# Performance work log

Hardware: AMD Instinct MI355X
Metric: run time of the kernel (lower is better)

## Reference

```python
import jax, jax.numpy as jnp
import numpy as np

B, C, W = 32, 3, 512
KSIZE = 5
EPS = 8.0
ID_OFFSET = 4.0
SCALE = ID_OFFSET / (W - 1)            # identity_offset / (image_crop - 1)
DEF_OFF = (2.0 + SCALE) / 2.0          # deforming_offset
PIX_W = 2.0 / W                        # pixel width in [-1,1] coords

def _gauss_kernel2d(k):
    sigma = k * 0.15 + 0.35
    half = (k - 1) * 0.5
    x = np.linspace(-half, half, k)
    pdf = np.exp(-0.5 * (x / sigma) ** 2)
    k1 = pdf / pdf.sum()
    return np.outer(k1, k1).astype(np.float32)

def _samp_iden():
    seq = np.arange(-(W - 1), W, 2) / (W - 1.0)   # length W, identity coords
    gx = np.tile(seq, (W, 1))
    gy = gx.T
    return jnp.asarray(np.stack([gx, gy])[None].astype(np.float32))  # [1,2,W,W]

IDEN = _samp_iden()
GKER = jnp.broadcast_to(jnp.asarray(_gauss_kernel2d(KSIZE))[None, None], (2, 1, KSIZE, KSIZE))

def _blur(g):
    p = KSIZE // 2
    g = jnp.pad(g, ((0, 0), (0, 0), (p, p), (p, p)), mode='reflect')
    # depthwise conv over the 2 grid channels (groups=2)
    return jax.lax.conv_general_dilated(g, GKER, (1, 1), 'VALID', feature_group_count=2)

def _forward_grid(prim_grid):
    pg = _blur(prim_grid)
    sg = pg + IDEN                                   # prim -> samp
    # samp -> accu: conv_transpose with [1,-1] == first difference (leading zero)
    s = sg + DEF_OFF
    sx, sy = s[:, :1], s[:, 1:2]
    ax = sx - jnp.concatenate([jnp.zeros_like(sx[..., :1]), sx[..., :-1]], axis=3)
    ay = sy - jnp.concatenate([jnp.zeros_like(sy[:, :, :1]), sy[:, :, :-1]], axis=2)
    ag = jnp.concatenate([ax, ay], axis=1) / SCALE
    ag = jax.nn.relu(ag)                             # accu_clip
    # accu -> samp: conv_transpose with all-ones filter == cumulative sum
    a = ag * SCALE
    sx2 = jnp.cumsum(a[:, :1], axis=3)
    sy2 = jnp.cumsum(a[:, 1:2], axis=2)
    sg = jnp.concatenate([sx2, sy2], axis=1) - DEF_OFF
    pg = jnp.clip(sg - IDEN, -PIX_W * EPS, PIX_W * EPS)  # prim_clip
    return jnp.clip(pg + IDEN, -1.0, 1.0)                # samp_clip (hardtanh)

def _grid_sample(img, grid):
    # img [B,C,W,W], grid [B,W,W,2] in [-1,1]; bilinear, zeros padding, align_corners=True
    x = (grid[..., 0] + 1.0) * 0.5 * (W - 1)
    y = (grid[..., 1] + 1.0) * 0.5 * (W - 1)
    x0 = jnp.floor(x); y0 = jnp.floor(y)
    x1 = x0 + 1.0;     y1 = y0 + 1.0
    wx1 = x - x0; wx0 = 1.0 - wx1
    wy1 = y - y0; wy0 = 1.0 - wy1
    def gather(xi, yi):
        valid = ((xi >= 0) & (xi < W) & (yi >= 0) & (yi < W)).astype(img.dtype)
        xc = jnp.clip(xi, 0, W - 1).astype(jnp.int32)
        yc = jnp.clip(yi, 0, W - 1).astype(jnp.int32)
        v = jax.vmap(lambda im, yy, xx: im[:, yy, xx])(img, yc, xc)  # [B,C,W,W]
        return v * valid[:, None]
    return (gather(x0, y0) * (wx0 * wy0)[:, None] + gather(x1, y0) * (wx1 * wy0)[:, None]
          + gather(x0, y1) * (wx0 * wy1)[:, None] + gather(x1, y1) * (wx1 * wy1)[:, None])

def setup_inputs() -> dict:
    key = jax.random.key(0)
    k1, k2 = jax.random.split(key)
    image = jax.random.normal(k1, (B, C, W, W), dtype=jnp.float32)
    prim_grid = jax.random.normal(k2, (B, 2, W, W), dtype=jnp.float32) * 0.01
    return {"image": image, "prim_grid": prim_grid}

def reference(image, prim_grid):
    samp_grid = _forward_grid(prim_grid)
    binding_grid = jnp.transpose(samp_grid, (0, 2, 3, 1))  # [B,W,W,2]
    return _grid_sample(image, binding_grid)
```

## Files before the change

kernel.cpp:

```cpp
#include <hip/hip_runtime.h>
#include <math.h>

#define WID 512
#define NB  32
#define NC  3
#define WW  (WID * WID)

constexpr float SCALE_F   = (float)(4.0 / 511.0);
constexpr float DEF_OFF_F = (float)((2.0 + 4.0 / 511.0) * 0.5);
constexpr float CLIP_F    = 0.03125f;

__device__ __forceinline__ int refl(int r) {
  r = r < 0 ? -r : r;
  return r > WID - 1 ? 2 * (WID - 1) - r : r;
}

__device__ __forceinline__ float seqf(int i) {
  return ((float)(2 * i - 511)) / 511.0f;
}

__device__ __forceinline__ void gl_lds16(const float* g, float* l) {
  __builtin_amdgcn_global_load_lds(
      (const __attribute__((address_space(1))) void*)g,
      (__attribute__((address_space(3))) void*)l, 16, 0, 0);
}

#define KY1_ROWS 133
#define KY1_COLS 72

__global__ __launch_bounds__(512)
void grid_kernel(const float* __restrict__ pg, float* __restrict__ gridx,
                 float* __restrict__ gridy, float* __restrict__ qsum,
                 float kw0, float kw1, float kw2) {
  if (blockIdx.x < 2048) {
    const int lane = threadIdx.x & 63;
    const int wv   = threadIdx.x >> 6;
    const int R = blockIdx.x * 8 + wv;
    const int b = R >> 9;
    const int i = R & (WID - 1);
    const float* base = pg + (size_t)b * 2 * WW;

    float v[8] = {0.f,0.f,0.f,0.f,0.f,0.f,0.f,0.f};
    const int rows[5] = {refl(i - 2), refl(i - 1), i, refl(i + 1), refl(i + 2)};
    const float wts[5] = {kw0, kw1, kw2, kw1, kw0};
#pragma unroll
    for (int r = 0; r < 5; ++r) {
      const float4* p = (const float4*)(base + (size_t)rows[r] * WID + lane * 8);
      float4 A = p[0], Bq = p[1];
      float w = wts[r];
      v[0] += w * A.x;  v[1] += w * A.y;  v[2] += w * A.z;  v[3] += w * A.w;
      v[4] += w * Bq.x; v[5] += w * Bq.y; v[6] += w * Bq.z; v[7] += w * Bq.w;
    }

    float em1 = __shfl_up(v[7], 1, 64);
    float em2 = __shfl_up(v[6], 1, 64);
    float ep8 = __shfl_down(v[0], 1, 64);
    float ep9 = __shfl_down(v[1], 1, 64);
    if (lane == 0)  { em1 = v[1]; em2 = v[2]; }
    if (lane == 63) { ep8 = v[6]; ep9 = v[5]; }

    float h[8];
    h[0] = kw2 * v[0] + kw1 * (em1 + v[1]) + kw0 * (em2 + v[2]);
    h[1] = kw2 * v[1] + kw1 * (v[0] + v[2]) + kw0 * (em1 + v[3]);
#pragma unroll
    for (int k = 2; k < 6; ++k)
      h[k] = kw2 * v[k] + kw1 * (v[k - 1] + v[k + 1]) + kw0 * (v[k - 2] + v[k + 2]);
    h[6] = kw2 * v[6] + kw1 * (v[5] + v[7]) + kw0 * (v[4] + ep8);
    h[7] = kw2 * v[7] + kw1 * (v[6] + ep8) + kw0 * (v[5] + ep9);

    float s[8], a[8], p[8];
#pragma unroll
    for (int k = 0; k < 8; ++k) s[k] = h[k] + seqf(lane * 8 + k) + DEF_OFF_F;

    float sm1 = __shfl_up(s[7], 1, 64);
    if (lane == 0) sm1 = 0.0f;
    a[0] = fmaxf((s[0] - sm1) / SCALE_F, 0.0f) * SCALE_F;
#pragma unroll
    for (int k = 1; k < 8; ++k)
      a[k] = fmaxf((s[k] - s[k - 1]) / SCALE_F, 0.0f) * SCALE_F;

    p[0] = a[0];
#pragma unroll
    for (int k = 1; k < 8; ++k) p[k] = p[k - 1] + a[k];
    float incl = p[7];
#pragma unroll
    for (int off = 1; off < 64; off <<= 1) {
      float n = __shfl_up(incl, off, 64);
      if (lane >= off) incl += n;
    }
    float excl = incl - p[7];

    float og[8];
#pragma unroll
    for (int k = 0; k < 8; ++k) {
      float gx = seqf(lane * 8 + k);
      float d = (p[k] + excl) - DEF_OFF_F - gx;
      d = fminf(fmaxf(d, -CLIP_F), CLIP_F);
      og[k] = fminf(fmaxf(d + gx, -1.0f), 1.0f);
    }
    float4* o = (float4*)(gridx + ((size_t)b * WID + i) * WID + lane * 8);
    o[0] = make_float4(og[0], og[1], og[2], og[3]);
    o[1] = make_float4(og[4], og[5], og[6], og[7]);
  } else {
    const int bid  = blockIdx.x - 2048;
    const int q    = bid & 3;
    const int tile = (bid >> 2) & 7;
    const int b    = bid >> 5;
    const int q0   = q << 7;
    const int gc0  = tile << 6;

    __shared__ float L[KY1_ROWS * KY1_COLS];
    __shared__ float ss[8][64];

    const float* src = pg + ((size_t)b * 2 + 1) * WW;
    for (int idx = threadIdx.x; idx < KY1_ROWS * 18; idx += 512) {
      int lr = idx / 18;
      int k  = idx - lr * 18;
      int gr = refl(q0 - 3 + lr);
      int gcb = gc0 - 4 + (k << 2);
      gcb = gcb < 0 ? 0 : (gcb > WID - 4 ? WID - 4 : gcb);
      float4 v = *(const float4*)(src + (size_t)gr * WID + gcb);
      *(float4*)(&L[lr * KY1_COLS + (k << 2)]) = v;
    }
    __syncthreads();

    const int j   = threadIdx.x & 63;
    const int seg = threadIdx.x >> 6;

    int jcc[5];
#pragma unroll
    for (int d = 0; d < 5; ++d)
      jcc[d] = refl(gc0 + j + d - 2) - gc0 + 4;

    auto HB = [&](int r) -> float {
      const float* Lr = &L[r * KY1_COLS];
      return kw2 * Lr[jcc[2]] + kw1 * (Lr[jcc[1]] + Lr[jcc[3]])
           + kw0 * (Lr[jcc[0]] + Lr[jcc[4]]);
    };

    const int lri0 = seg * 16 + 2;
    float hm2 = HB(lri0 - 2);
    float hm1 = HB(lri0 - 1);
    float hc  = HB(lri0);
    float hp1 = HB(lri0 + 1);
    float hp2 = HB(lri0 + 2);

    const int istart = q0 + seg * 16 - 1;
    float areg[16];
    float sprev = 0.0f, suma = 0.0f;
#pragma unroll
    for (int k = 0; k <= 16; ++k) {
      float blur = kw2 * hc + kw1 * (hm1 + hp1) + kw0 * (hm2 + hp2);
      float s = blur + seqf(istart + k) + DEF_OFF_F;
      if (k == 0) {
        sprev = (q == 0 && seg == 0) ? 0.0f : s;
      } else {
        float a = fmaxf((s - sprev) / SCALE_F, 0.0f) * SCALE_F;
        areg[k - 1] = a;
        suma += a;
        sprev = s;
      }
      if (k < 16) {
        hm2 = hm1; hm1 = hc; hc = hp1; hp1 = hp2;
        hp2 = HB(lri0 + k + 3);
      }
    }

    ss[seg][j] = suma;
    __syncthreads();
    float off = 0.0f;
#pragma unroll
    for (int w = 0; w < 7; ++w)
      if (w < seg) off += ss[w][j];
    if (seg == 7)
      qsum[((size_t)b * 4 + q) * WID + gc0 + j] = off + suma;

    float* ob = gridy + (size_t)b * WW + (size_t)(q0 + seg * 16) * WID + gc0 + j;
    float cum = off;
#pragma unroll
    for (int k = 0; k < 16; ++k) {
      cum += areg[k];
      ob[(size_t)k * WID] = cum;
    }
  }
}

__global__ __launch_bounds__(128)
void ky2_kernel(float* __restrict__ gridy, const float* __restrict__ qsum) {
  const int b = blockIdx.x >> 9;
  const int i = blockIdx.x & 511;
  const int q = i >> 7;
  const int j4 = threadIdx.x << 2;
  const float* qs = qsum + (size_t)b * 4 * WID + j4;
  float ox = 0.f, oy = 0.f, oz = 0.f, ow = 0.f;
  for (int w = 0; w < q; ++w) {
    float4 t = *(const float4*)(qs + (size_t)w * WID);
    ox += t.x; oy += t.y; oz += t.z; ow += t.w;
  }
  const float gy = seqf(i);
  float* p = gridy + ((size_t)b * WID + i) * WID + j4;
  float4 v = *(float4*)p;
  auto fin = [&](float c) -> float {
    float d = c - DEF_OFF_F - gy;
    d = fminf(fmaxf(d, -CLIP_F), CLIP_F);
    return fminf(fmaxf(d + gy, -1.0f), 1.0f);
  };
  v.x = fin(v.x + ox); v.y = fin(v.y + oy);
  v.z = fin(v.z + oz); v.w = fin(v.w + ow);
  *(float4*)p = v;
}

#define STILE  16
#define SROWS  32
#define SAMP_BLOCKS (NB * NC * (WID / STILE))

template<bool FUSEY>
__global__ __launch_bounds__(1024, 8)
void sample_kernel(const float* __restrict__ img, const float* __restrict__ gridx,
                   const float* __restrict__ gridy, const float* __restrict__ qsum,
                   float* __restrict__ out) {
  const int nb = (blockIdx.x & 7) * (SAMP_BLOCKS / 8) + (blockIdx.x >> 3);
  const int rt = nb & 31;
  const int bc = nb >> 5;
  const int b  = bc / 3;
  const int c  = bc - b * 3;
  const int r0 = rt * STILE;

  __shared__ float tile[SROWS * WID];

  const float* ic = img + ((size_t)b * NC + c) * WW;
#pragma unroll
  for (int it = 0; it < 4; ++it) {
    int chunk = it * 1024 + threadIdx.x;
    int lr = chunk >> 7;
    int c4 = (chunk & 127) << 2;
    int gr = r0 - 8 + lr;
    gr = gr < 0 ? 0 : (gr > WID - 1 ? WID - 1 : gr);
    gl_lds16(ic + (size_t)gr * WID + c4, &tile[lr * WID + c4]);
  }
  __syncthreads();

  const int j    = threadIdx.x & 511;
  const int rsub = (threadIdx.x >> 9) << 3;

  float offy = 0.0f;
  if (FUSEY) {
    const int q = r0 >> 7;
    const float* qs = qsum + (size_t)b * 4 * WID + j;
    for (int w = 0; w < q; ++w) offy += qs[(size_t)w * WID];
  }

  float* ob = out + ((size_t)b * NC + c) * WW;
#pragma unroll
  for (int r = 0; r < 8; ++r) {
    const int i = r0 + rsub + r;
    const size_t gidx = ((size_t)b * WID + i) * WID + j;
    float gx = gridx[gidx];
    float gy = gridy[gidx];
    if (FUSEY) {
      const float gyl = seqf(i);
      float d = (gy + offy) - DEF_OFF_F - gyl;
      d = fminf(fmaxf(d, -CLIP_F), CLIP_F);
      gy = fminf(fmaxf(d + gyl, -1.0f), 1.0f);
    }
    float x = (gx + 1.0f) * (0.5f * (float)(WID - 1));
    float y = (gy + 1.0f) * (0.5f * (float)(WID - 1));
    float x0f = floorf(x), y0f = floorf(y);
    int x0 = (int)x0f, y0 = (int)y0f;
    float wx1 = x - x0f, wx0 = 1.0f - wx1;
    float wy1 = y - y0f, wy0 = 1.0f - wy1;
    int x1 = x0 + 1, y1 = y0 + 1;
    int x1c = x1 > WID - 1 ? WID - 1 : x1;
    int y1c = y1 > WID - 1 ? WID - 1 : y1;
    float vx1 = x1 < WID ? 1.0f : 0.0f;
    float vy1 = y1 < WID ? 1.0f : 0.0f;

    float w00 = wx0 * wy0;
    float w01 = wx1 * wy0 * vx1;
    float w10 = wx0 * wy1 * vy1;
    float w11 = wx1 * wy1 * vx1 * vy1;

    int ly0 = y0 - r0 + 8;
    int ly1 = y1c - r0 + 8;
    float v00 = tile[ly0 * WID + x0];
    float v01 = tile[ly0 * WID + x1c];
    float v10 = tile[ly1 * WID + x0];
    float v11 = tile[ly1 * WID + x1c];

    ob[(size_t)i * WID + j] = w00 * v00 + w01 * v01 + w10 * v10 + w11 * v11;
  }
}

extern "C" void kernel_launch(void* const* d_in, const int* in_sizes, int n_in,
                              void* d_out, int out_size, void* d_ws, size_t ws_size,
                              hipStream_t stream) {
  const float* img = (const float*)d_in[0];
  const float* pg  = (const float*)d_in[1];
  float* out = (float*)d_out;

  float* gridx = (float*)d_ws;
  float* gridy = gridx + (size_t)NB * WW;

  const size_t grids_bytes = (size_t)2 * NB * WW * sizeof(float);
  const size_t qsum_bytes  = (size_t)NB * 4 * WID * sizeof(float);
  const bool ws_fits = (ws_size >= grids_bytes + qsum_bytes);
  float* qsum = ws_fits ? (float*)((char*)d_ws + grids_bytes)
                        : (float*)d_out;

  double sigma = 5.0 * 0.15 + 0.35;
  double p0 = exp(-0.5 * (2.0 / sigma) * (2.0 / sigma));
  double p1 = exp(-0.5 * (1.0 / sigma) * (1.0 / sigma));
  double p2 = 1.0;
  double sum = 2.0 * p0 + 2.0 * p1 + p2;
  float kw0 = (float)(p0 / sum), kw1 = (float)(p1 / sum), kw2 = (float)(p2 / sum);

  grid_kernel<<<2048 + NB * 32, 512, 0, stream>>>(pg, gridx, gridy, qsum,
                                                  kw0, kw1, kw2);
  if (ws_fits) {
    sample_kernel<true><<<SAMP_BLOCKS, 1024, 0, stream>>>(img, gridx, gridy,
                                                          qsum, out);
  } else {
    ky2_kernel<<<NB * WID, 128, 0, stream>>>(gridy, qsum);
    sample_kernel<false><<<SAMP_BLOCKS, 1024, 0, stream>>>(img, gridx, gridy,
                                                           qsum, out);
  }
}
```

Before: 261.0 us.

## Simplify arithmetic, async-load blur tiles, prefetch grids before barrier, lerp sampling

Drops the redundant divide and multiply by SCALE around the relu and rewrites seqf as an fma. The blur-y tile load now uses global_load_lds instead of register round-trips. In the sampler, grid values and the qsum offset are loaded before the LDS barrier so their latency overlaps the tile fill. Bilinear interpolation becomes two nested lerps with clamped index offsets. The x1/y1 edge handling and the scale and fma changes may shift floating-point results slightly.

```diff
diff --git a/kernel.cpp b/kernel.cpp
--- a/kernel.cpp
+++ b/kernel.cpp
@@ -16,7 +16,7 @@
 }
 
 __device__ __forceinline__ float seqf(int i) {
-  return ((float)(2 * i - 511)) / 511.0f;
+  return fmaf((float)i, 2.0f / 511.0f, -1.0f);
 }
 
 __device__ __forceinline__ void gl_lds16(const float* g, float* l) {
@@ -74,10 +74,10 @@
 
     float sm1 = __shfl_up(s[7], 1, 64);
     if (lane == 0) sm1 = 0.0f;
-    a[0] = fmaxf((s[0] - sm1) / SCALE_F, 0.0f) * SCALE_F;
+    a[0] = fmaxf(s[0] - sm1, 0.0f);
 #pragma unroll
     for (int k = 1; k < 8; ++k)
-      a[k] = fmaxf((s[k] - s[k - 1]) / SCALE_F, 0.0f) * SCALE_F;
+      a[k] = fmaxf(s[k] - s[k - 1], 0.0f);
 
     p[0] = a[0];
 #pragma unroll
@@ -113,14 +113,16 @@
     __shared__ float ss[8][64];
 
     const float* src = pg + ((size_t)b * 2 + 1) * WW;
-    for (int idx = threadIdx.x; idx < KY1_ROWS * 18; idx += 512) {
-      int lr = idx / 18;
-      int k  = idx - lr * 18;
-      int gr = refl(q0 - 3 + lr);
-      int gcb = gc0 - 4 + (k << 2);
-      gcb = gcb < 0 ? 0 : (gcb > WID - 4 ? WID - 4 : gcb);
-      float4 v = *(const float4*)(src + (size_t)gr * WID + gcb);
-      *(float4*)(&L[lr * KY1_COLS + (k << 2)]) = v;
+    {
+      float* lbase = &L[0];
+      for (int idx = threadIdx.x; idx < KY1_ROWS * 18; idx += 512) {
+        int lr = idx / 18;
+        int k  = idx - lr * 18;
+        int gr = refl(q0 - 3 + lr);
+        int gcb = gc0 - 4 + (k << 2);
+        gcb = gcb < 0 ? 0 : (gcb > WID - 4 ? WID - 4 : gcb);
+        gl_lds16(src + (size_t)gr * WID + gcb, lbase + (idx << 2));
+      }
     }
     __syncthreads();
 
@@ -155,7 +157,7 @@
       if (k == 0) {
         sprev = (q == 0 && seg == 0) ? 0.0f : s;
       } else {
-        float a = fmaxf((s - sprev) / SCALE_F, 0.0f) * SCALE_F;
+        float a = fmaxf(s - sprev, 0.0f);
         areg[k - 1] = a;
         suma += a;
         sprev = s;
@@ -236,30 +238,39 @@
     int c4 = (chunk & 127) << 2;
     int gr = r0 - 8 + lr;
     gr = gr < 0 ? 0 : (gr > WID - 1 ? WID - 1 : gr);
-    gl_lds16(ic + (size_t)gr * WID + c4, &tile[lr * WID + c4]);
-  }
-  __syncthreads();
-
-  const int j    = threadIdx.x & 511;
-  const int rsub = (threadIdx.x >> 9) << 3;
-
-  float offy = 0.0f;
+    gl_lds16(ic + (size_t)gr * WID + c4, &tile[chunk << 2]);
+  }
+
+  const int j     = threadIdx.x & 511;
+  const int rsub  = (threadIdx.x >> 9) << 3;
+  const int ibase = r0 + rsub;
+
+  const float* gxp = gridx + ((size_t)b * WID + ibase) * WID + j;
+  const float* gyp = gridy + ((size_t)b * WID + ibase) * WID + j;
+  float gxv[8], gyv[8];
+#pragma unroll
+  for (int r = 0; r < 8; ++r) {
+    gxv[r] = gxp[(size_t)r * WID];
+    gyv[r] = gyp[(size_t)r * WID];
+  }
+  float offc = -DEF_OFF_F;
   if (FUSEY) {
     const int q = r0 >> 7;
     const float* qs = qsum + (size_t)b * 4 * WID + j;
-    for (int w = 0; w < q; ++w) offy += qs[(size_t)w * WID];
-  }
+    for (int w = 0; w < q; ++w) offc += qs[(size_t)w * WID];
+  }
+
+  __syncthreads();
 
   float* ob = out + ((size_t)b * NC + c) * WW;
 #pragma unroll
   for (int r = 0; r < 8; ++r) {
-    const int i = r0 + rsub + r;
-    const size_t gidx = ((size_t)b * WID + i) * WID + j;
-    float gx = gridx[gidx];
-    float gy = gridy[gidx];
+    const int i = ibase + r;
+    float gx = gxv[r];
+    float gy = gyv[r];
     if (FUSEY) {
       const float gyl = seqf(i);
-      float d = (gy + offy) - DEF_OFF_F - gyl;
+      float d = (gy + offc) - gyl;
       d = fminf(fmaxf(d, -CLIP_F), CLIP_F);
       gy = fminf(fmaxf(d + gyl, -1.0f), 1.0f);
     }
@@ -267,27 +278,20 @@
     float y = (gy + 1.0f) * (0.5f * (float)(WID - 1));
     float x0f = floorf(x), y0f = floorf(y);
     int x0 = (int)x0f, y0 = (int)y0f;
-    float wx1 = x - x0f, wx0 = 1.0f - wx1;
-    float wy1 = y - y0f, wy0 = 1.0f - wy1;
-    int x1 = x0 + 1, y1 = y0 + 1;
-    int x1c = x1 > WID - 1 ? WID - 1 : x1;
-    int y1c = y1 > WID - 1 ? WID - 1 : y1;
-    float vx1 = x1 < WID ? 1.0f : 0.0f;
-    float vy1 = y1 < WID ? 1.0f : 0.0f;
-
-    float w00 = wx0 * wy0;
-    float w01 = wx1 * wy0 * vx1;
-    float w10 = wx0 * wy1 * vy1;
-    float w11 = wx1 * wy1 * vx1 * vy1;
-
-    int ly0 = y0 - r0 + 8;
-    int ly1 = y1c - r0 + 8;
-    float v00 = tile[ly0 * WID + x0];
-    float v01 = tile[ly0 * WID + x1c];
-    float v10 = tile[ly1 * WID + x0];
-    float v11 = tile[ly1 * WID + x1c];
-
-    ob[(size_t)i * WID + j] = w00 * v00 + w01 * v01 + w10 * v10 + w11 * v11;
+    float wx1 = x - x0f;
+    float wy1 = y - y0f;
+    int dx = x0 < WID - 1 ? 1 : 0;
+    int dy = y0 < WID - 1 ? WID : 0;
+    int i00 = ((y0 - r0 + 8) << 9) + x0;
+
+    float v00 = tile[i00];
+    float v01 = tile[i00 + dx];
+    float v10 = tile[i00 + dy];
+    float v11 = tile[i00 + dy + dx];
+
+    float top = v00 + wx1 * (v01 - v00);
+    float bot = v10 + wx1 * (v11 - v10);
+    ob[(size_t)i * WID + j] = top + wy1 * (bot - top);
   }
 }
 
```

Result: faster. 254.0 us (-2.7%).
